# Kernel optimization log

Measured on AMD Instinct MI355X. Metric: run time of the kernel, lower is better.

Reference implementation:

```python
import jax, jax.numpy as jnp
import numpy as np

D_MODEL = 1024
H = 16
D_K = D_MODEL // H
D_FF = 4096
EPS = 1e-6


def layer_norm(x, alpha, bias):
    mean = jnp.mean(x, axis=-1, keepdims=True)
    var = jnp.mean((x - mean) ** 2, axis=-1, keepdims=True)  # unbiased=False
    return alpha * (x - mean) / jnp.sqrt(var + EPS) + bias


def setup_inputs() -> dict:
    key = jax.random.key(0)
    ks = jax.random.split(key, 8)
    B, S = 4, 2048
    sd = 1.0 / np.sqrt(D_MODEL)
    x = jax.random.normal(ks[0], (B, S, D_MODEL), dtype=jnp.float32)
    src_mask = jnp.ones((B, 1, S), dtype=jnp.int32)
    wq = jax.random.normal(ks[1], (D_MODEL, D_MODEL), jnp.float32) * sd
    wk = jax.random.normal(ks[2], (D_MODEL, D_MODEL), jnp.float32) * sd
    wv = jax.random.normal(ks[3], (D_MODEL, D_MODEL), jnp.float32) * sd
    wo = jax.random.normal(ks[4], (D_MODEL, D_MODEL), jnp.float32) * sd
    w1 = jax.random.normal(ks[5], (D_FF, D_MODEL), jnp.float32) * sd
    b1 = jnp.zeros((D_FF,), jnp.float32)
    w2 = jax.random.normal(ks[6], (D_MODEL, D_FF), jnp.float32) * (1.0 / np.sqrt(D_FF))
    b2 = jnp.zeros((D_MODEL,), jnp.float32)
    ln1_a = jnp.ones((D_MODEL,), jnp.float32)
    ln1_b = jnp.zeros((D_MODEL,), jnp.float32)
    ln2_a = jnp.ones((D_MODEL,), jnp.float32)
    ln2_b = jnp.zeros((D_MODEL,), jnp.float32)
    return dict(x=x, src_mask=src_mask, wq=wq, wk=wk, wv=wv, wo=wo,
                ln1_a=ln1_a, ln1_b=ln1_b, ln2_a=ln2_a, ln2_b=ln2_b,
                w1=w1, b1=b1, w2=w2, b2=b2)


def attention(xn, wq, wk, wv, wo, src_mask):
    B, S, _ = xn.shape
    # torch nn.Linear: y = x @ W.T
    q = (xn @ wq.T).reshape(B, S, H, D_K).transpose(0, 2, 1, 3)  # [B,H,S,Dk]
    k = (xn @ wk.T).reshape(B, S, H, D_K).transpose(0, 2, 1, 3)
    v = (xn @ wv.T).reshape(B, S, H, D_K).transpose(0, 2, 1, 3)
    scores = jnp.einsum('bhqd,bhkd->bhqk', q, k) / np.sqrt(D_K)
    m = src_mask[:, None, :, :]  # [B,1,1,S] from [B,1,S]
    scores = jnp.where(m == 0, -jnp.inf, scores)
    attn = jax.nn.softmax(scores, axis=-1)
    out = jnp.einsum('bhqk,bhkd->bhqd', attn, v)
    out = out.transpose(0, 2, 1, 3).reshape(B, S, D_MODEL)
    return out @ wo.T


def reference(x, src_mask, wq, wk, wv, wo, ln1_a, ln1_b, ln2_a, ln2_b, w1, b1, w2, b2):
    # pre-LN residual 1: self-attention
    xn = layer_norm(x, ln1_a, ln1_b)
    x = x + attention(xn, wq, wk, wv, wo, src_mask)
    # pre-LN residual 2: FFN
    xn = layer_norm(x, ln2_a, ln2_b)
    h = jax.nn.relu(xn @ w1.T + b1)
    x = x + (h @ w2.T + b2)
    return x
```

## Files before the change

kernel.cpp:

```cpp
#include <hip/hip_runtime.h>
#include <stdint.h>

typedef unsigned short u16;
typedef __bf16 bf16x8 __attribute__((ext_vector_type(8)));
typedef float   f32x4 __attribute__((ext_vector_type(4)));
typedef u16     u16x8 __attribute__((ext_vector_type(8)));
typedef u16     u16x4 __attribute__((ext_vector_type(4)));

__device__ __forceinline__ u16 f2bf(float f) {
    union { float f; uint32_t i; } c; c.f = f;
    uint32_t r = c.i + 0x7FFFu + ((c.i >> 16) & 1u);
    return (u16)(r >> 16);
}
__device__ __forceinline__ uint32_t cvt_pk_bf16(float lo, float hi) {
    uint32_t r;
    asm("v_cvt_pk_bf16_f32 %0, %1, %2" : "=v"(r) : "v"(lo), "v"(hi));
    return r;
}
__device__ __forceinline__ void gload_lds16(const u16* g, u16* l) {
    __builtin_amdgcn_global_load_lds(
        (__attribute__((address_space(1))) void*)(g),
        (__attribute__((address_space(3))) void*)(l), 16, 0, 0);
}
template<int N>
__device__ __forceinline__ void wait_vm_barrier() {
    asm volatile("s_waitcnt vmcnt(%0)\n\ts_barrier" :: "n"(N) : "memory");
}

__global__ __launch_bounds__(256) void cvt_all(
    const float* __restrict__ wq, const float* __restrict__ wk,
    const float* __restrict__ wv, const float* __restrict__ wo,
    const float* __restrict__ w1, const float* __restrict__ w2,
    u16* __restrict__ wqb, u16* __restrict__ wkb, u16* __restrict__ wvb,
    u16* __restrict__ wob, u16* __restrict__ w1b, u16* __restrict__ w2b)
{
    int blk = blockIdx.x;
    const float* src; u16* dst; int off;
    if      (blk < 1024)  { src = wq; dst = wqb; off = blk; }
    else if (blk < 2048)  { src = wk; dst = wkb; off = blk - 1024; }
    else if (blk < 3072)  { src = wv; dst = wvb; off = blk - 2048; }
    else if (blk < 4096)  { src = wo; dst = wob; off = blk - 3072; }
    else if (blk < 8192)  { src = w1; dst = w1b; off = blk - 4096; }
    else                  { src = w2; dst = w2b; off = blk - 8192; }
    int i = off * 1024 + threadIdx.x * 4;
    float4 v = *(const float4*)(src + i);
    u16x4 o; o[0] = f2bf(v.x); o[1] = f2bf(v.y); o[2] = f2bf(v.z); o[3] = f2bf(v.w);
    *(u16x4*)(dst + i) = o;
}

__global__ __launch_bounds__(256) void ln_kernel(
    const float* __restrict__ x, const float* __restrict__ ga,
    const float* __restrict__ be, u16* __restrict__ out)
{
    const int D = 1024;
    int row  = blockIdx.x * 4 + (threadIdx.x >> 6);
    int lane = threadIdx.x & 63;
    const float* xr = x + (size_t)row * D + lane * 16;
    float f[16];
#pragma unroll
    for (int i = 0; i < 4; ++i) *(float4*)&f[i * 4] = *(const float4*)(xr + i * 4);
    float s = 0.f, s2 = 0.f;
#pragma unroll
    for (int i = 0; i < 16; ++i) { s += f[i]; s2 += f[i] * f[i]; }
#pragma unroll
    for (int off = 1; off < 64; off <<= 1) {
        s  += __shfl_xor(s,  off, 64);
        s2 += __shfl_xor(s2, off, 64);
    }
    float mean = s * (1.0f / 1024.0f);
    float var  = s2 * (1.0f / 1024.0f) - mean * mean;
    var = var < 0.f ? 0.f : var;
    float inv = 1.0f / sqrtf(var + 1e-6f);
    float g[16], b[16];
#pragma unroll
    for (int i = 0; i < 4; ++i) {
        *(float4*)&g[i * 4] = *(const float4*)(ga + lane * 16 + i * 4);
        *(float4*)&b[i * 4] = *(const float4*)(be + lane * 16 + i * 4);
    }
    u16x8 o0, o1;
#pragma unroll
    for (int i = 0; i < 8; ++i) {
        o0[i] = f2bf(g[i]     * (f[i]     - mean) * inv + b[i]);
        o1[i] = f2bf(g[8 + i] * (f[8 + i] - mean) * inv + b[8 + i]);
    }
    u16* orow = out + (size_t)row * D + lane * 16;
    *(u16x8*)(orow)     = o0;
    *(u16x8*)(orow + 8) = o1;
}


__device__ __forceinline__ void gemm_ring256_core(
    const u16* __restrict__ A, const u16* __restrict__ W,
    int K, int ldw, int row_a0, int row_w0,
    u16* smem, f32x4 (&acc)[8][4])
{
    int tid  = threadIdx.x;
    int lane = tid & 63;
    int quad = lane >> 4, l16 = lane & 15;
    int wave = tid >> 6;
    int wm = wave >> 2, wn = wave & 3;

    int srow = tid >> 2, scol = (tid & 3) * 8;
    const u16* a0 = A + (size_t)(row_a0 + srow) * K + scol;
    const u16* a1 = a0 + (size_t)128 * K;
    const u16* b0 = W + (size_t)(row_w0 + srow) * ldw + scol;
    const u16* b1 = b0 + (size_t)128 * ldw;
    u16* dst = smem + tid * 8;
    const int nk = K >> 5;

#pragma unroll
    for (int s = 0; s < 3; ++s) {
        u16* d = dst + s * 16384;
        const int k = s * 32;
        gload_lds16(a0 + k, d);
        gload_lds16(a1 + k, d + 4096);
        gload_lds16(b0 + k, d + 8192);
        gload_lds16(b1 + k, d + 12288);
    }
    const int abase = wm * 4096 + l16 * 32 + quad * 8;
    const int bbase = 8192 + (wn >> 1) * 4096 + ((wn & 1) * 64 + l16) * 32 + quad * 8;

    wait_vm_barrier<8>();

    for (int t = 0; t < nk; ++t) {
        if (t + 3 < nk) {
            u16* d = dst + ((t + 3) & 3) * 16384;
            const int k = (t + 3) * 32;
            gload_lds16(a0 + k, d);
            gload_lds16(a1 + k, d + 4096);
            gload_lds16(b0 + k, d + 8192);
            gload_lds16(b1 + k, d + 12288);
        }
        const u16* buf = smem + (t & 3) * 16384;
        bf16x8 af[8], bf[4];
#pragma unroll
        for (int mt = 0; mt < 8; ++mt)
            af[mt] = *(const bf16x8*)(&buf[abase + mt * 512]);
#pragma unroll
        for (int nt = 0; nt < 4; ++nt)
            bf[nt] = *(const bf16x8*)(&buf[bbase + nt * 512]);
#pragma unroll
        for (int mt = 0; mt < 8; ++mt)
#pragma unroll
            for (int nt = 0; nt < 4; ++nt)
                acc[mt][nt] = __builtin_amdgcn_mfma_f32_16x16x32_bf16(
                    af[mt], bf[nt], acc[mt][nt], 0, 0, 0);
        if      (t + 3 < nk) wait_vm_barrier<8>();
        else if (t + 2 < nk) wait_vm_barrier<4>();
        else if (t + 1 < nk) wait_vm_barrier<0>();
    }
}

__device__ __forceinline__ void gemm_ring128_core(
    const u16* __restrict__ A, const u16* __restrict__ W,
    int K, int ldw, int row_a0, int row_w0,
    u16* smem, f32x4 (&acc)[4][4])
{
    int tid  = threadIdx.x;
    int lane = tid & 63;
    int quad = lane >> 4, l16 = lane & 15;
    int wave = tid >> 6;
    int wm = wave >> 2, wn = wave & 3;

    int srow = tid >> 2, scol = (tid & 3) * 8;
    const u16* a0 = A + (size_t)(row_a0 + srow) * K + scol;
    const u16* b0 = W + (size_t)(row_w0 + srow) * ldw + scol;
    const u16* b1 = b0 + (size_t)128 * ldw;
    u16* dst = smem + tid * 8;
    const int nk = K >> 5;

#pragma unroll
    for (int s = 0; s < 3; ++s) {
        u16* d = dst + s * 12288;
        const int k = s * 32;
        gload_lds16(a0 + k, d);
        gload_lds16(b0 + k, d + 4096);
        gload_lds16(b1 + k, d + 8192);
    }
    const int abase = (wm * 64 + l16) * 32 + quad * 8;
    const int bbase = 4096 + (wn >> 1) * 4096 + ((wn & 1) * 64 + l16) * 32 + quad * 8;

    wait_vm_barrier<6>();

    for (int t = 0; t < nk; ++t) {
        if (t + 3 < nk) {
            u16* d = dst + ((t + 3) & 3) * 12288;
            const int k = (t + 3) * 32;
            gload_lds16(a0 + k, d);
            gload_lds16(b0 + k, d + 4096);
            gload_lds16(b1 + k, d + 8192);
        }
        const u16* buf = smem + (t & 3) * 12288;
        bf16x8 af[4], bf[4];
#pragma unroll
        for (int mt = 0; mt < 4; ++mt)
            af[mt] = *(const bf16x8*)(&buf[abase + mt * 512]);
#pragma unroll
        for (int nt = 0; nt < 4; ++nt)
            bf[nt] = *(const bf16x8*)(&buf[bbase + nt * 512]);
#pragma unroll
        for (int mt = 0; mt < 4; ++mt)
#pragma unroll
            for (int nt = 0; nt < 4; ++nt)
                acc[mt][nt] = __builtin_amdgcn_mfma_f32_16x16x32_bf16(
                    af[mt], bf[nt], acc[mt][nt], 0, 0, 0);
        if      (t + 3 < nk) wait_vm_barrier<6>();
        else if (t + 2 < nk) wait_vm_barrier<3>();
        else if (t + 1 < nk) wait_vm_barrier<0>();
    }
}

template<bool OUTF32>
__global__ __launch_bounds__(512, 2) void gemm256sq(
    const u16* __restrict__ A, const u16* __restrict__ W,
    const float* __restrict__ bias, const float* __restrict__ resid,
    void* __restrict__ Cp, int M, int N, int K, int ldw, int do_relu)
{
    __shared__ u16 smem[65536];
    int tid  = threadIdx.x;
    int lane = tid & 63, wave = tid >> 6;
    int quad = lane >> 4, l16 = lane & 15;
    int wm = wave >> 2, wn = wave & 3;
    const int row_a0 = blockIdx.x * 256, row_w0 = blockIdx.y * 256;
    f32x4 acc[8][4] = {};
    gemm_ring256_core(A, W, K, ldw, row_a0, row_w0, smem, acc);
#pragma unroll
    for (int mt = 0; mt < 8; ++mt) {
#pragma unroll
        for (int nt = 0; nt < 4; ++nt) {
#pragma unroll
            for (int r = 0; r < 4; ++r) {
                int grow = row_a0 + wm * 128 + mt * 16 + quad * 4 + r;
                int gcol = row_w0 + wn * 64 + nt * 16 + l16;
                float vv = acc[mt][nt][r];
                if (bias)    vv += bias[gcol];
                if (do_relu) vv = vv > 0.f ? vv : 0.f;
                if (resid)   vv += resid[(size_t)grow * N + gcol];
                if (OUTF32) ((float*)Cp)[(size_t)grow * N + gcol] = vv;
                else        ((u16*)Cp)[(size_t)grow * N + gcol] = f2bf(vv);
            }
        }
    }
}

__global__ __launch_bounds__(512, 2) void gemm256sq_qkv(
    const u16* __restrict__ A, const u16* __restrict__ Wqkv,
    u16* __restrict__ qo, u16* __restrict__ ko, u16* __restrict__ vo, int K)
{
    __shared__ u16 smem[65536];
    int tid  = threadIdx.x;
    int lane = tid & 63, wave = tid >> 6;
    int quad = lane >> 4, l16 = lane & 15;
    int wm = wave >> 2, wn = wave & 3;
    const int row_a0 = blockIdx.x * 256, row_w0 = blockIdx.y * 256;
    f32x4 acc[8][4] = {};
    gemm_ring256_core(A, Wqkv, K, K, row_a0, row_w0, smem, acc);
    int seg = row_w0 >> 10;
    u16* dst = (seg == 0) ? qo : (seg == 1) ? ko : vo;
    int col0 = row_w0 & 1023;
#pragma unroll
    for (int mt = 0; mt < 8; ++mt) {
#pragma unroll
        for (int nt = 0; nt < 4; ++nt) {
#pragma unroll
            for (int r = 0; r < 4; ++r) {
                int grow = row_a0 + wm * 128 + mt * 16 + quad * 4 + r;
                int gcol = col0 + wn * 64 + nt * 16 + l16;
                dst[(size_t)grow * 1024 + gcol] = f2bf(acc[mt][nt][r]);
            }
        }
    }
}

template<bool OUTF32>
__global__ __launch_bounds__(512, 2) void gemm128x256(
    const u16* __restrict__ A, const u16* __restrict__ W,
    const float* __restrict__ bias, const float* __restrict__ resid,
    void* __restrict__ Cp, int M, int N, int K, int ldw, int do_relu)
{
    __shared__ u16 smem[49152];
    int tid  = threadIdx.x;
    int lane = tid & 63, wave = tid >> 6;
    int quad = lane >> 4, l16 = lane & 15;
    int wm = wave >> 2, wn = wave & 3;
    const int row_a0 = blockIdx.x * 128, row_w0 = blockIdx.y * 256;
    f32x4 acc[4][4] = {};
    gemm_ring128_core(A, W, K, ldw, row_a0, row_w0, smem, acc);
#pragma unroll
    for (int mt = 0; mt < 4; ++mt) {
#pragma unroll
        for (int nt = 0; nt < 4; ++nt) {
#pragma unroll
            for (int r = 0; r < 4; ++r) {
                int grow = row_a0 + wm * 64 + mt * 16 + quad * 4 + r;
                int gcol = row_w0 + wn * 64 + nt * 16 + l16;
                float vv = acc[mt][nt][r];
                if (bias)    vv += bias[gcol];
                if (do_relu) vv = vv > 0.f ? vv : 0.f;
                if (resid)   vv += resid[(size_t)grow * N + gcol];
                if (OUTF32) ((float*)Cp)[(size_t)grow * N + gcol] = vv;
                else        ((u16*)Cp)[(size_t)grow * N + gcol] = f2bf(vv);
            }
        }
    }
}

__global__ __launch_bounds__(512, 4) void attn_kernel(
    const u16* __restrict__ Q, const u16* __restrict__ Km, const u16* __restrict__ Vm,
    const int* __restrict__ mask, u16* __restrict__ O)
{
    const int S = 2048, DM = 1024;
    const float C1 = 0.18033688f;
    const float C0 = -11.541560f;
    __shared__ u16 smem[35840];
    u16* Ks0 = smem;
    u16* Ks1 = smem + 4096;
    u16* Vt0 = smem + 8192;
    u16* Vt1 = smem + 12800;
    u16* Ps  = smem + 17408;
    u16* Qs  = smem + 17408;

    int qt = blockIdx.x, bh = blockIdx.y;
    int b = bh >> 4, h = bh & 15;
    int tid = threadIdx.x;
    int wave = tid >> 6, lane = tid & 63;
    int quad = lane >> 4, l16 = lane & 15;
    size_t base = (size_t)b * S;
    size_t hoff = (size_t)h * 64;

    {
        int r = tid >> 1, c0 = (tid & 1) * 32;
        const u16* src = Q + (base + qt * 256 + r) * DM + hoff + c0;
        u16* dq = Qs + r * 72 + c0;
        *(u16x8*)(dq)      = *(const u16x8*)(src);
        *(u16x8*)(dq + 8)  = *(const u16x8*)(src + 8);
        *(u16x8*)(dq + 16) = *(const u16x8*)(src + 16);
        *(u16x8*)(dq + 24) = *(const u16x8*)(src + 24);
    }
    const u16* ksrc = Km + (base + (tid >> 3)) * DM + hoff
                    + ((tid & 7) ^ ((tid >> 5) & 7)) * 8;
    int kp = tid & 31, d0 = (tid >> 5) * 4;
    const u16* vsrc = Vm + (base + kp * 2) * DM + hoff + d0;
    const int* msrc = mask + b * S + 4 * l16;

    __syncthreads();
    const int q0 = wave * 32;
    bf16x8 qf00 = *(const bf16x8*)(&Qs[(q0 + l16) * 72 + quad * 8]);
    bf16x8 qf01 = *(const bf16x8*)(&Qs[(q0 + l16) * 72 + 32 + quad * 8]);
    bf16x8 qf10 = *(const bf16x8*)(&Qs[(q0 + 16 + l16) * 72 + quad * 8]);
    bf16x8 qf11 = *(const bf16x8*)(&Qs[(q0 + 16 + l16) * 72 + 32 + quad * 8]);
    const int swz = (l16 & 7) * 8;
    const int u0  = (quad * 8) ^ swz;

    {
        u16x4 va = *(const u16x4*)(vsrc);
        u16x4 vb = *(const u16x4*)(vsrc + DM);
        gload_lds16(ksrc, Ks0 + tid * 8);
        ksrc += 64 * DM; vsrc += 64 * DM;
#pragma unroll
        for (int i = 0; i < 4; ++i) {
            uint32_t w = (uint32_t)va[i] | ((uint32_t)vb[i] << 16);
            *(uint32_t*)(&Vt0[(d0 + i) * 72 + kp * 2]) = w;
        }
    }
    __syncthreads();

    float l0[4] = {0.f, 0.f, 0.f, 0.f};
    float l1[4] = {0.f, 0.f, 0.f, 0.f};
    f32x4 o0[4] = {}, o1[4] = {};

    for (int it = 0; it < 32; ++it) {
        const u16* Kcur = (it & 1) ? Ks1 : Ks0;
        const u16* Vcur = (it & 1) ? Vt1 : Vt0;
        u16* Knxt = (it & 1) ? Ks0 : Ks1;
        u16* Vnxt = (it & 1) ? Vt0 : Vt1;
        const bool pfch = (it < 31);
        u16x4 va, vb;
        if (pfch) {
            va = *(const u16x4*)(vsrc);
            vb = *(const u16x4*)(vsrc + DM);
            gload_lds16(ksrc, Knxt + tid * 8);
            ksrc += 64 * DM; vsrc += 64 * DM;
        }
        f32x4 s0[4] = {}, s1[4] = {};
#pragma unroll
        for (int t = 0; t < 4; ++t) {
            const u16* krp = Kcur + (4 * l16 + t) * 64;
            bf16x8 kf0 = *(const bf16x8*)(krp + u0);
            bf16x8 kf1 = *(const bf16x8*)(krp + (u0 ^ 32));
            s0[t] = __builtin_amdgcn_mfma_f32_16x16x32_bf16(qf00, kf0, s0[t], 0, 0, 0);
            s0[t] = __builtin_amdgcn_mfma_f32_16x16x32_bf16(qf01, kf1, s0[t], 0, 0, 0);
            s1[t] = __builtin_amdgcn_mfma_f32_16x16x32_bf16(qf10, kf0, s1[t], 0, 0, 0);
            s1[t] = __builtin_amdgcn_mfma_f32_16x16x32_bf16(qf11, kf1, s1[t], 0, 0, 0);
        }
        int4 mk4 = *(const int4*)(msrc); msrc += 64;
        float c0t[4];
        c0t[0] = (mk4.x == 0) ? -1e38f : C0;
        c0t[1] = (mk4.y == 0) ? -1e38f : C0;
        c0t[2] = (mk4.z == 0) ? -1e38f : C0;
        c0t[3] = (mk4.w == 0) ? -1e38f : C0;
#pragma unroll
        for (int r = 0; r < 4; ++r) {
            float p0 = exp2f(fmaf(s0[0][r], C1, c0t[0]));
            float p1 = exp2f(fmaf(s0[1][r], C1, c0t[1]));
            float p2 = exp2f(fmaf(s0[2][r], C1, c0t[2]));
            float p3 = exp2f(fmaf(s0[3][r], C1, c0t[3]));
            l0[r] += (p0 + p1) + (p2 + p3);
            uint2 pw;
            pw.x = cvt_pk_bf16(p0, p1);
            pw.y = cvt_pk_bf16(p2, p3);
            *(uint2*)(&Ps[(q0 + quad * 4 + r) * 72 + 4 * l16]) = pw;
        }
#pragma unroll
        for (int r = 0; r < 4; ++r) {
            float p0 = exp2f(fmaf(s1[0][r], C1, c0t[0]));
            float p1 = exp2f(fmaf(s1[1][r], C1, c0t[1]));
            float p2 = exp2f(fmaf(s1[2][r], C1, c0t[2]));
            float p3 = exp2f(fmaf(s1[3][r], C1, c0t[3]));
            l1[r] += (p0 + p1) + (p2 + p3);
            uint2 pw;
            pw.x = cvt_pk_bf16(p0, p1);
            pw.y = cvt_pk_bf16(p2, p3);
            *(uint2*)(&Ps[(q0 + 16 + quad * 4 + r) * 72 + 4 * l16]) = pw;
        }
        bf16x8 pf00 = *(const bf16x8*)(&Ps[(q0 + l16) * 72 + quad * 8]);
        bf16x8 pf01 = *(const bf16x8*)(&Ps[(q0 + l16) * 72 + 32 + quad * 8]);
        bf16x8 pf10 = *(const bf16x8*)(&Ps[(q0 + 16 + l16) * 72 + quad * 8]);
        bf16x8 pf11 = *(const bf16x8*)(&Ps[(q0 + 16 + l16) * 72 + 32 + quad * 8]);
#pragma unroll
        for (int t = 0; t < 4; ++t) {
            bf16x8 vf0 = *(const bf16x8*)(&Vcur[(t * 16 + l16) * 72 + quad * 8]);
            bf16x8 vf1 = *(const bf16x8*)(&Vcur[(t * 16 + l16) * 72 + 32 + quad * 8]);
            o0[t] = __builtin_amdgcn_mfma_f32_16x16x32_bf16(pf00, vf0, o0[t], 0, 0, 0);
            o0[t] = __builtin_amdgcn_mfma_f32_16x16x32_bf16(pf01, vf1, o0[t], 0, 0, 0);
            o1[t] = __builtin_amdgcn_mfma_f32_16x16x32_bf16(pf10, vf0, o1[t], 0, 0, 0);
            o1[t] = __builtin_amdgcn_mfma_f32_16x16x32_bf16(pf11, vf1, o1[t], 0, 0, 0);
        }
        if (pfch) {
#pragma unroll
            for (int i = 0; i < 4; ++i) {
                uint32_t w = (uint32_t)va[i] | ((uint32_t)vb[i] << 16);
                *(uint32_t*)(&Vnxt[(d0 + i) * 72 + kp * 2]) = w;
            }
        }
        __syncthreads();
    }
#pragma unroll
    for (int r = 0; r < 4; ++r) {
#pragma unroll
        for (int off = 1; off < 16; off <<= 1) {
            l0[r] += __shfl_xor(l0[r], off, 16);
            l1[r] += __shfl_xor(l1[r], off, 16);
        }
        float i0 = 1.0f / l0[r];
        float i1 = 1.0f / l1[r];
        u16* dst0 = O + (base + qt * 256 + q0 + quad * 4 + r) * DM + hoff + l16;
        u16* dst1 = dst0 + (size_t)16 * DM;
#pragma unroll
        for (int t = 0; t < 4; ++t) {
            dst0[t * 16] = f2bf(o0[t][r] * i0);
            dst1[t * 16] = f2bf(o1[t][r] * i1);
        }
    }
}

extern "C" void kernel_launch(void* const* d_in, const int* in_sizes, int n_in,
                              void* d_out, int out_size, void* d_ws, size_t ws_size,
                              hipStream_t stream)
{
    (void)in_sizes; (void)n_in; (void)out_size; (void)ws_size;
    const float* x    = (const float*)d_in[0];
    const int*   mask = (const int*)d_in[1];
    const float* wq   = (const float*)d_in[2];
    const float* wk   = (const float*)d_in[3];
    const float* wv   = (const float*)d_in[4];
    const float* wo   = (const float*)d_in[5];
    const float* ln1a = (const float*)d_in[6];
    const float* ln1b = (const float*)d_in[7];
    const float* ln2a = (const float*)d_in[8];
    const float* ln2b = (const float*)d_in[9];
    const float* w1   = (const float*)d_in[10];
    const float* b1   = (const float*)d_in[11];
    const float* w2   = (const float*)d_in[12];
    const float* b2   = (const float*)d_in[13];

    const int M = 8192, D = 1024, F = 4096;
    char* ws = (char*)d_ws;
    u16*  wqkv = (u16*)(ws);
    u16*  wqb = wqkv;
    u16*  wkb = (u16*)(ws + (2u  << 20));
    u16*  wvb = (u16*)(ws + (4u  << 20));
    u16*  wob = (u16*)(ws + (6u  << 20));
    u16*  w1b = (u16*)(ws + (8u  << 20));
    u16*  w2b = (u16*)(ws + (16u << 20));
    u16*  xn  = (u16*)(ws + (24u << 20));
    u16*  q   = (u16*)(ws + (40u << 20));
    u16*  hb  = (u16*)(ws + (40u << 20));

    u16*   kbuf = (u16*)d_out;
    u16*   vbuf = (u16*)d_out + (size_t)M * D;
    float* x1   = (float*)d_out;

    cvt_all<<<12288, 256, 0, stream>>>(wq, wk, wv, wo, w1, w2,
                                       wqb, wkb, wvb, wob, w1b, w2b);

    ln_kernel<<<M / 4, 256, 0, stream>>>(x, ln1a, ln1b, xn);
    dim3 gq(M / 256, 3072 / 256);
    gemm256sq_qkv<<<gq, 512, 0, stream>>>(xn, wqkv, q, kbuf, vbuf, D);
    dim3 ga(2048 / 256, 64);
    attn_kernel<<<ga, 512, 0, stream>>>(q, kbuf, vbuf, mask, xn);
    dim3 g1(M / 128, D / 256);
    gemm128x256<true ><<<g1, 512, 0, stream>>>(xn, wob, nullptr, x, x1, M, D, D, D, 0);
    ln_kernel<<<M / 4, 256, 0, stream>>>(x1, ln2a, ln2b, xn);
    dim3 gf1(M / 256, 2048 / 256);
    dim3 gf2(M / 128, D / 256);
    gemm256sq<false><<<gf1, 512, 0, stream>>>(xn, w1b, b1, nullptr, hb, M, 2048, D, D, 1);
    gemm128x256<true ><<<gf2, 512, 0, stream>>>(hb, w2b, nullptr, x1, x1, M, D, 2048, F, 0);
    gemm256sq<false><<<gf1, 512, 0, stream>>>(xn, w1b + (size_t)2048 * D, b1 + 2048, nullptr, hb, M, 2048, D, D, 1);
    gemm128x256<true ><<<gf2, 512, 0, stream>>>(hb, w2b + 2048, b2, x1, x1, M, D, 2048, F, 0);
}
```

Before: 588.3 us.

## Split 256-tile GEMM loop into prioritized MFMA phases and shrink N=1024 GEMM tiles

The 256x256 GEMM core now splits each k-step into two MFMA halves. Global-to-LDS prefetches are interleaved between them, with extra barriers and s_setprio raising wave priority during the MFMA bursts, so memory issue overlaps compute. The 128x256 GEMM used for the output projection and FFN down-projection is replaced by a 128x128 tile with a 3-stage ring and less LDS, allowing 4 blocks per CU and twice as many blocks for better occupancy on N=1024 outputs. The trade-offs are more barriers per k-step and lower data reuse per tile.

```diff
diff --git a/kernel.cpp b/kernel.cpp
--- a/kernel.cpp
+++ b/kernel.cpp
@@ -25,6 +25,9 @@
 template<int N>
 __device__ __forceinline__ void wait_vm_barrier() {
     asm volatile("s_waitcnt vmcnt(%0)\n\ts_barrier" :: "n"(N) : "memory");
+}
+__device__ __forceinline__ void sbar() {
+    asm volatile("s_barrier" ::: "memory");
 }
 
 __global__ __launch_bounds__(256) void cvt_all(
@@ -88,8 +91,7 @@
     *(u16x8*)(orow + 8) = o1;
 }
 
-
-__device__ __forceinline__ void gemm_ring256_core(
+__device__ __forceinline__ void gemm256p_core(
     const u16* __restrict__ A, const u16* __restrict__ W,
     int K, int ldw, int row_a0, int row_w0,
     u16* smem, f32x4 (&acc)[8][4])
@@ -111,107 +113,60 @@
 #pragma unroll
     for (int s = 0; s < 3; ++s) {
         u16* d = dst + s * 16384;
-        const int k = s * 32;
-        gload_lds16(a0 + k, d);
-        gload_lds16(a1 + k, d + 4096);
-        gload_lds16(b0 + k, d + 8192);
-        gload_lds16(b1 + k, d + 12288);
+        gload_lds16(a0 + s * 32, d);
+        gload_lds16(a1 + s * 32, d + 4096);
+        gload_lds16(b0 + s * 32, d + 8192);
+        gload_lds16(b1 + s * 32, d + 12288);
     }
     const int abase = wm * 4096 + l16 * 32 + quad * 8;
     const int bbase = 8192 + (wn >> 1) * 4096 + ((wn & 1) * 64 + l16) * 32 + quad * 8;
-
     wait_vm_barrier<8>();
 
     for (int t = 0; t < nk; ++t) {
-        if (t + 3 < nk) {
-            u16* d = dst + ((t + 3) & 3) * 16384;
-            const int k = (t + 3) * 32;
-            gload_lds16(a0 + k, d);
-            gload_lds16(a1 + k, d + 4096);
-            gload_lds16(b0 + k, d + 8192);
-            gload_lds16(b1 + k, d + 12288);
-        }
         const u16* buf = smem + (t & 3) * 16384;
-        bf16x8 af[8], bf[4];
-#pragma unroll
-        for (int mt = 0; mt < 8; ++mt)
+        u16* nd = dst + ((t + 3) & 3) * 16384;
+        const bool pf = (t + 3 < nk);
+        const int k3 = (t + 3) * 32;
+        bf16x8 af[4], bf[4];
+#pragma unroll
+        for (int mt = 0; mt < 4; ++mt)
             af[mt] = *(const bf16x8*)(&buf[abase + mt * 512]);
 #pragma unroll
         for (int nt = 0; nt < 4; ++nt)
             bf[nt] = *(const bf16x8*)(&buf[bbase + nt * 512]);
-#pragma unroll
-        for (int mt = 0; mt < 8; ++mt)
+        if (pf) { gload_lds16(a0 + k3, nd); gload_lds16(a1 + k3, nd + 4096); }
+        sbar();
+        __builtin_amdgcn_s_setprio(1);
+#pragma unroll
+        for (int mt = 0; mt < 4; ++mt)
 #pragma unroll
             for (int nt = 0; nt < 4; ++nt)
                 acc[mt][nt] = __builtin_amdgcn_mfma_f32_16x16x32_bf16(
                     af[mt], bf[nt], acc[mt][nt], 0, 0, 0);
-        if      (t + 3 < nk) wait_vm_barrier<8>();
+        __builtin_amdgcn_s_setprio(0);
+        sbar();
+        bf16x8 ag[4];
+#pragma unroll
+        for (int mt = 0; mt < 4; ++mt)
+            ag[mt] = *(const bf16x8*)(&buf[abase + (mt + 4) * 512]);
+        if (pf) { gload_lds16(b0 + k3, nd + 8192); gload_lds16(b1 + k3, nd + 12288); }
+        sbar();
+        __builtin_amdgcn_s_setprio(1);
+#pragma unroll
+        for (int mt = 0; mt < 4; ++mt)
+#pragma unroll
+            for (int nt = 0; nt < 4; ++nt)
+                acc[mt + 4][nt] = __builtin_amdgcn_mfma_f32_16x16x32_bf16(
+                    ag[mt], bf[nt], acc[mt + 4][nt], 0, 0, 0);
+        __builtin_amdgcn_s_setprio(0);
+        if      (pf)         wait_vm_barrier<8>();
         else if (t + 2 < nk) wait_vm_barrier<4>();
         else if (t + 1 < nk) wait_vm_barrier<0>();
     }
 }
 
-__device__ __forceinline__ void gemm_ring128_core(
-    const u16* __restrict__ A, const u16* __restrict__ W,
-    int K, int ldw, int row_a0, int row_w0,
-    u16* smem, f32x4 (&acc)[4][4])
-{
-    int tid  = threadIdx.x;
-    int lane = tid & 63;
-    int quad = lane >> 4, l16 = lane & 15;
-    int wave = tid >> 6;
-    int wm = wave >> 2, wn = wave & 3;
-
-    int srow = tid >> 2, scol = (tid & 3) * 8;
-    const u16* a0 = A + (size_t)(row_a0 + srow) * K + scol;
-    const u16* b0 = W + (size_t)(row_w0 + srow) * ldw + scol;
-    const u16* b1 = b0 + (size_t)128 * ldw;
-    u16* dst = smem + tid * 8;
-    const int nk = K >> 5;
-
-#pragma unroll
-    for (int s = 0; s < 3; ++s) {
-        u16* d = dst + s * 12288;
-        const int k = s * 32;
-        gload_lds16(a0 + k, d);
-        gload_lds16(b0 + k, d + 4096);
-        gload_lds16(b1 + k, d + 8192);
-    }
-    const int abase = (wm * 64 + l16) * 32 + quad * 8;
-    const int bbase = 4096 + (wn >> 1) * 4096 + ((wn & 1) * 64 + l16) * 32 + quad * 8;
-
-    wait_vm_barrier<6>();
-
-    for (int t = 0; t < nk; ++t) {
-        if (t + 3 < nk) {
-            u16* d = dst + ((t + 3) & 3) * 12288;
-            const int k = (t + 3) * 32;
-            gload_lds16(a0 + k, d);
-            gload_lds16(b0 + k, d + 4096);
-            gload_lds16(b1 + k, d + 8192);
-        }
-        const u16* buf = smem + (t & 3) * 12288;
-        bf16x8 af[4], bf[4];
-#pragma unroll
-        for (int mt = 0; mt < 4; ++mt)
-            af[mt] = *(const bf16x8*)(&buf[abase + mt * 512]);
-#pragma unroll
-        for (int nt = 0; nt < 4; ++nt)
-            bf[nt] = *(const bf16x8*)(&buf[bbase + nt * 512]);
-#pragma unroll
-        for (int mt = 0; mt < 4; ++mt)
-#pragma unroll
-            for (int nt = 0; nt < 4; ++nt)
-                acc[mt][nt] = __builtin_amdgcn_mfma_f32_16x16x32_bf16(
-                    af[mt], bf[nt], acc[mt][nt], 0, 0, 0);
-        if      (t + 3 < nk) wait_vm_barrier<6>();
-        else if (t + 2 < nk) wait_vm_barrier<3>();
-        else if (t + 1 < nk) wait_vm_barrier<0>();
-    }
-}
-
 template<bool OUTF32>
-__global__ __launch_bounds__(512, 2) void gemm256sq(
+__global__ __launch_bounds__(512, 2) void gemm256p(
     const u16* __restrict__ A, const u16* __restrict__ W,
     const float* __restrict__ bias, const float* __restrict__ resid,
     void* __restrict__ Cp, int M, int N, int K, int ldw, int do_relu)
@@ -223,7 +178,7 @@
     int wm = wave >> 2, wn = wave & 3;
     const int row_a0 = blockIdx.x * 256, row_w0 = blockIdx.y * 256;
     f32x4 acc[8][4] = {};
-    gemm_ring256_core(A, W, K, ldw, row_a0, row_w0, smem, acc);
+    gemm256p_core(A, W, K, ldw, row_a0, row_w0, smem, acc);
 #pragma unroll
     for (int mt = 0; mt < 8; ++mt) {
 #pragma unroll
@@ -243,7 +198,7 @@
     }
 }
 
-__global__ __launch_bounds__(512, 2) void gemm256sq_qkv(
+__global__ __launch_bounds__(512, 2) void gemm256p_qkv(
     const u16* __restrict__ A, const u16* __restrict__ Wqkv,
     u16* __restrict__ qo, u16* __restrict__ ko, u16* __restrict__ vo, int K)
 {
@@ -254,7 +209,7 @@
     int wm = wave >> 2, wn = wave & 3;
     const int row_a0 = blockIdx.x * 256, row_w0 = blockIdx.y * 256;
     f32x4 acc[8][4] = {};
-    gemm_ring256_core(A, Wqkv, K, K, row_a0, row_w0, smem, acc);
+    gemm256p_core(A, Wqkv, K, K, row_a0, row_w0, smem, acc);
     int seg = row_w0 >> 10;
     u16* dst = (seg == 0) ? qo : (seg == 1) ? ko : vo;
     int col0 = row_w0 & 1023;
@@ -272,28 +227,80 @@
     }
 }
 
+__device__ __forceinline__ void gemm128q_core(
+    const u16* __restrict__ A, const u16* __restrict__ W,
+    int K, int ldw, int row_a0, int row_w0,
+    u16* smem, f32x4 (&acc)[4][2])
+{
+    int tid  = threadIdx.x;
+    int lane = tid & 63;
+    int quad = lane >> 4, l16 = lane & 15;
+    int wave = tid >> 6;
+    int wm = wave >> 2, wn = wave & 3;
+
+    const u16* a0 = A + (size_t)(row_a0 + (tid >> 2)) * K   + (tid & 3) * 8;
+    const u16* b0 = W + (size_t)(row_w0 + (tid >> 2)) * ldw + (tid & 3) * 8;
+    u16* dst = smem + tid * 8;
+    const int nk = K >> 5;
+
+#pragma unroll
+    for (int s = 0; s < 3; ++s) {
+        gload_lds16(a0 + s * 32, dst + s * 8192);
+        gload_lds16(b0 + s * 32, dst + s * 8192 + 4096);
+    }
+    const int abase = (wm * 64 + l16) * 32 + quad * 8;
+    const int bbase = 4096 + (wn * 32 + l16) * 32 + quad * 8;
+    wait_vm_barrier<4>();
+
+    int cb = 0, nb = 16384;
+    for (int t = 0; t < nk; ++t) {
+        if (t + 2 < nk) {
+            gload_lds16(a0 + (t + 2) * 32, dst + nb);
+            gload_lds16(b0 + (t + 2) * 32, dst + nb + 4096);
+        }
+        const u16* buf = smem + cb;
+        bf16x8 af[4], bf[2];
+#pragma unroll
+        for (int mt = 0; mt < 4; ++mt)
+            af[mt] = *(const bf16x8*)(&buf[abase + mt * 512]);
+#pragma unroll
+        for (int nt = 0; nt < 2; ++nt)
+            bf[nt] = *(const bf16x8*)(&buf[bbase + nt * 512]);
+#pragma unroll
+        for (int mt = 0; mt < 4; ++mt)
+#pragma unroll
+            for (int nt = 0; nt < 2; ++nt)
+                acc[mt][nt] = __builtin_amdgcn_mfma_f32_16x16x32_bf16(
+                    af[mt], bf[nt], acc[mt][nt], 0, 0, 0);
+        if      (t + 2 < nk) wait_vm_barrier<2>();
+        else if (t + 1 < nk) wait_vm_barrier<0>();
+        cb = (cb == 16384) ? 0 : cb + 8192;
+        nb = (nb == 16384) ? 0 : nb + 8192;
+    }
+}
+
 template<bool OUTF32>
-__global__ __launch_bounds__(512, 2) void gemm128x256(
+__global__ __launch_bounds__(512, 4) void gemm128q(
     const u16* __restrict__ A, const u16* __restrict__ W,
     const float* __restrict__ bias, const float* __restrict__ resid,
     void* __restrict__ Cp, int M, int N, int K, int ldw, int do_relu)
 {
-    __shared__ u16 smem[49152];
+    __shared__ u16 smem[24576];
     int tid  = threadIdx.x;
     int lane = tid & 63, wave = tid >> 6;
     int quad = lane >> 4, l16 = lane & 15;
     int wm = wave >> 2, wn = wave & 3;
-    const int row_a0 = blockIdx.x * 128, row_w0 = blockIdx.y * 256;
-    f32x4 acc[4][4] = {};
-    gemm_ring128_core(A, W, K, ldw, row_a0, row_w0, smem, acc);
+    const int row_a0 = blockIdx.x * 128, row_w0 = blockIdx.y * 128;
+    f32x4 acc[4][2] = {};
+    gemm128q_core(A, W, K, ldw, row_a0, row_w0, smem, acc);
 #pragma unroll
     for (int mt = 0; mt < 4; ++mt) {
 #pragma unroll
-        for (int nt = 0; nt < 4; ++nt) {
+        for (int nt = 0; nt < 2; ++nt) {
 #pragma unroll
             for (int r = 0; r < 4; ++r) {
                 int grow = row_a0 + wm * 64 + mt * 16 + quad * 4 + r;
-                int gcol = row_w0 + wn * 64 + nt * 16 + l16;
+                int gcol = row_w0 + wn * 32 + nt * 16 + l16;
                 float vv = acc[mt][nt][r];
                 if (bias)    vv += bias[gcol];
                 if (do_relu) vv = vv > 0.f ? vv : 0.f;
@@ -506,16 +513,16 @@
 
     ln_kernel<<<M / 4, 256, 0, stream>>>(x, ln1a, ln1b, xn);
     dim3 gq(M / 256, 3072 / 256);
-    gemm256sq_qkv<<<gq, 512, 0, stream>>>(xn, wqkv, q, kbuf, vbuf, D);
+    gemm256p_qkv<<<gq, 512, 0, stream>>>(xn, wqkv, q, kbuf, vbuf, D);
     dim3 ga(2048 / 256, 64);
     attn_kernel<<<ga, 512, 0, stream>>>(q, kbuf, vbuf, mask, xn);
-    dim3 g1(M / 128, D / 256);
-    gemm128x256<true ><<<g1, 512, 0, stream>>>(xn, wob, nullptr, x, x1, M, D, D, D, 0);
+    dim3 g1(M / 128, D / 128);
+    gemm128q<true ><<<g1, 512, 0, stream>>>(xn, wob, nullptr, x, x1, M, D, D, D, 0);
     ln_kernel<<<M / 4, 256, 0, stream>>>(x1, ln2a, ln2b, xn);
     dim3 gf1(M / 256, 2048 / 256);
-    dim3 gf2(M / 128, D / 256);
-    gemm256sq<false><<<gf1, 512, 0, stream>>>(xn, w1b, b1, nullptr, hb, M, 2048, D, D, 1);
-    gemm128x256<true ><<<gf2, 512, 0, stream>>>(hb, w2b, nullptr, x1, x1, M, D, 2048, F, 0);
-    gemm256sq<false><<<gf1, 512, 0, stream>>>(xn, w1b + (size_t)2048 * D, b1 + 2048, nullptr, hb, M, 2048, D, D, 1);
-    gemm128x256<true ><<<gf2, 512, 0, stream>>>(hb, w2b + 2048, b2, x1, x1, M, D, 2048, F, 0);
-}
+    dim3 gf2(M / 128, D / 128);
+    gemm256p<false><<<gf1, 512, 0, stream>>>(xn, w1b, b1, nullptr, hb, M, 2048, D, D, 1);
+    gemm128q<true ><<<gf2, 512, 0, stream>>>(hb, w2b, nullptr, x1, x1, M, D, 2048, F, 0);
+    gemm256p<false><<<gf1, 512, 0, stream>>>(xn, w1b + (size_t)2048 * D, b1 + 2048, nullptr, hb, M, 2048, D, D, 1);
+    gemm128q<true ><<<gf2, 512, 0, stream>>>(hb, w2b + 2048, b2, x1, x1, M, D, 2048, F, 0);
+}
```

New measurement: 579.0 us. Within noise of the previous version (-1.6%).
